# Optimization experiments

Hardware: AMD Instinct MI355X
Metric: run time of the kernel (lower is better)

The kernel has to match this reference:

```python
import jax, jax.numpy as jnp
import numpy as np

TOPK = 300
NUM_LEVELS = 3
GATE_TEMP = 1.0


def _normalized_grid(h, w):
    # matches torch: linspace(-1,1) meshgrid 'ij', stack (xx, yy) -> [h*w, 2]
    y = jnp.linspace(-1.0, 1.0, h, dtype=jnp.float32)
    x = jnp.linspace(-1.0, 1.0, w, dtype=jnp.float32)
    yy, xx = jnp.meshgrid(y, x, indexing='ij')
    return jnp.stack((xx, yy), axis=-1).reshape(h * w, 2)


def setup_inputs() -> dict:
    key = jax.random.key(0)
    ks = jax.random.split(key, 10)
    C, H_DIM, MAXL = 256, 256, 8
    shapes = [(8, C, 100, 152), (8, C, 50, 76), (8, C, 25, 38)]
    inp = {}
    for i, s in enumerate(shapes):
        inp[f'f{i}'] = jax.random.normal(ks[i], s, dtype=jnp.float32)
    inp['conv_w'] = jax.random.normal(ks[3], (C,), dtype=jnp.float32) * (1.0 / np.sqrt(C))
    inp['conv_b'] = jnp.zeros((1,), dtype=jnp.float32)
    inp['level_emb'] = jax.random.normal(ks[4], (MAXL, H_DIM), dtype=jnp.float32)
    qin = C + H_DIM + 3  # 515
    inp['w1'] = jax.random.normal(ks[5], (qin, H_DIM), dtype=jnp.float32) * (1.0 / np.sqrt(qin))
    inp['b1'] = jnp.zeros((H_DIM,), dtype=jnp.float32)
    inp['w2'] = jax.random.normal(ks[6], (H_DIM, H_DIM), dtype=jnp.float32) * (1.0 / np.sqrt(H_DIM))
    inp['b2'] = jnp.zeros((H_DIM,), dtype=jnp.float32)
    inp['gate_w'] = jax.random.normal(ks[7], (H_DIM, MAXL), dtype=jnp.float32) * (1.0 / np.sqrt(H_DIM))
    inp['gate_b'] = jnp.zeros((MAXL,), dtype=jnp.float32)
    inp['residual_scale'] = jnp.zeros((1,), dtype=jnp.float32)  # residual_scale_init=0.0
    return inp


def reference(f0, f1, f2, conv_w, conv_b, level_emb, w1, b1, w2, b2, gate_w, gate_b, residual_scale):
    levels = [f0, f1, f2]
    B = f0.shape[0]
    tok_s, tok_f, tok_p, tok_l = [], [], [], []
    for i, f in enumerate(levels):
        _, C, H, W = f.shape
        # 1x1 conv proxy objectness score -> [B, H*W]
        s = jnp.einsum('bchw,c->bhw', f, conv_w).reshape(B, H * W) + conv_b[0]
        tok_s.append(s)
        tok_f.append(f.reshape(B, C, H * W).transpose(0, 2, 1))       # [B, HW, C]
        tok_p.append(jnp.broadcast_to(_normalized_grid(H, W), (B, H * W, 2)))
        tok_l.append(jnp.full((B, H * W), i, dtype=jnp.int32))
    scores = jnp.concatenate(tok_s, axis=1)   # [B, N]
    feats = jnp.concatenate(tok_f, axis=1)    # [B, N, C]
    pos = jnp.concatenate(tok_p, axis=1)      # [B, N, 2]
    lvl = jnp.concatenate(tok_l, axis=1)      # [B, N]

    top_vals, top_idx = jax.lax.top_k(scores, TOPK)                     # [B, K]
    fk = jnp.take_along_axis(feats, top_idx[:, :, None], axis=1)        # [B, K, C]
    pk = jnp.take_along_axis(pos, top_idx[:, :, None], axis=1)          # [B, K, 2]
    lk = jnp.take_along_axis(lvl, top_idx, axis=1)                      # [B, K]
    sp = jax.nn.sigmoid(top_vals)                                       # [B, K]

    q = jnp.concatenate([fk, level_emb[lk], pk, sp[..., None]], axis=-1)  # [B, K, C+H+3]
    h = jax.nn.relu(q @ w1 + b1)
    h = jax.nn.relu(h @ w2 + b2)
    logits = (h @ gate_w + gate_b)[..., :NUM_LEVELS]                     # [B, K, L]
    gates = jax.nn.softmax(logits / GATE_TEMP, axis=-1)
    alpha = gates.mean(axis=1)                                           # [B, L]
    scale = 1.0 + residual_scale[0] * alpha                              # [B, L]

    outs = [f * scale[:, i][:, None, None, None] for i, f in enumerate(levels)]
    # flatten the output feature dict into one [B, sum(C*H*W)] array
    return jnp.concatenate([o.reshape(B, -1) for o in outs], axis=1)
```

## Files before the change

kernel.cpp:

```cpp
#include <hip/hip_runtime.h>
#include <hip/hip_bf16.h>

#define NTOK 19950
#define KTOP 300
#define NB 8
#define NQ (NB * KTOP)
#define QDIM 520

typedef float f32x4 __attribute__((ext_vector_type(4)));

__device__ __forceinline__ uint32_t fkey(float f) {
    uint32_t u = __float_as_uint(f);
    return (u & 0x80000000u) ? ~u : (u | 0x80000000u);
}

__global__ __launch_bounds__(256) void score_kernel(
    const float* __restrict__ f0, const float* __restrict__ f1, const float* __restrict__ f2,
    const float* __restrict__ conv_w, const float* __restrict__ conv_b,
    float* __restrict__ scores)
{
    __shared__ float cw[256];
    cw[threadIdx.x] = conv_w[threadIdx.x];
    __syncthreads();
    int t = blockIdx.x * 256 + threadIdx.x;
    if (t >= NB * NTOK) return;
    int b = t / NTOK;
    int pos = t - b * NTOK;
    const float* f; int HWl, hw;
    if (pos < 15200)      { f = f0; HWl = 15200; hw = pos; }
    else if (pos < 19000) { f = f1; HWl = 3800;  hw = pos - 15200; }
    else                  { f = f2; HWl = 950;   hw = pos - 19000; }
    const float* base = f + (size_t)b * 256 * HWl + hw;
    float s = 0.0f;
    #pragma unroll 16
    for (int c = 0; c < 256; ++c) s += base[(size_t)c * HWl] * cw[c];
    scores[t] = s + conv_b[0];
}

__global__ __launch_bounds__(1024, 1) void topk_kernel(
    const float* __restrict__ scores, int* __restrict__ top_idx)
{
    __shared__ uint32_t key[NTOK];
    __shared__ int whist[16][256];
    __shared__ int suffix[256];
    __shared__ uint32_t s_prefix;
    __shared__ int s_Kr, s_cnt, s_tcnt;
    __shared__ int tie[1024];
    const int tid = threadIdx.x;
    const int wv = tid >> 6;
    const int b = blockIdx.x;
    const float* srow = scores + b * NTOK;
    for (int i = tid; i < NTOK; i += 1024) key[i] = fkey(srow[i]);
    if (tid == 0) { s_prefix = 0u; s_Kr = KTOP; }
    __syncthreads();
    uint32_t pmask = 0u;
    for (int pass = 0; pass < 4; ++pass) {
        const int shift = 24 - 8 * pass;
        for (int i = tid; i < 16 * 256; i += 1024) ((int*)whist)[i] = 0;
        __syncthreads();
        const uint32_t prefix = s_prefix;
        const int Kr = s_Kr;
        for (int i = tid; i < NTOK; i += 1024) {
            uint32_t k = key[i];
            if ((k & pmask) == prefix) atomicAdd(&whist[wv][(k >> shift) & 255], 1);
        }
        __syncthreads();
        if (tid < 256) {
            int s = 0;
            #pragma unroll
            for (int w = 0; w < 16; ++w) s += whist[w][tid];
            suffix[tid] = s;
        }
        __syncthreads();
        for (int off = 1; off < 256; off <<= 1) {
            int t = 0;
            if (tid < 256 && tid + off < 256) t = suffix[tid + off];
            __syncthreads();
            if (tid < 256) suffix[tid] += t;
            __syncthreads();
        }
        if (tid < 256) {
            int sgeq = suffix[tid];
            int sgt  = (tid < 255) ? suffix[tid + 1] : 0;
            if (sgeq >= Kr && sgt < Kr) {
                s_prefix = prefix | ((uint32_t)tid << shift);
                s_Kr = Kr - sgt;
            }
        }
        __syncthreads();
        pmask |= (0xFFu << shift);
    }
    const uint32_t T = s_prefix;
    const int need = s_Kr;
    if (tid == 0) { s_cnt = 0; s_tcnt = 0; }
    __syncthreads();
    for (int i = tid; i < NTOK; i += 1024) {
        uint32_t k = key[i];
        if (k > T) {
            int p = atomicAdd(&s_cnt, 1);
            top_idx[b * KTOP + p] = i;
        } else if (k == T) {
            int p = atomicAdd(&s_tcnt, 1);
            if (p < 1024) tie[p] = i;
        }
    }
    __syncthreads();
    if (tid == 0) {
        int base = s_cnt;
        int tcnt = s_tcnt > 1024 ? 1024 : s_tcnt;
        for (int s = 0; s < need; ++s) {
            int mi = s;
            for (int u = s + 1; u < tcnt; ++u) if (tie[u] < tie[mi]) mi = u;
            int tmp = tie[s]; tie[s] = tie[mi]; tie[mi] = tmp;
            top_idx[b * KTOP + base + s] = tie[s];
        }
    }
}

__global__ __launch_bounds__(256) void gather_kernel(
    const float* __restrict__ f0, const float* __restrict__ f1, const float* __restrict__ f2,
    const float* __restrict__ scores, const int* __restrict__ top_idx,
    const float* __restrict__ level_emb, float* __restrict__ Q)
{
    const int k = blockIdx.x;
    const int b = k / KTOP;
    const int idx = top_idx[k];
    int lvl, hw, HWl, Wl, Hl;
    if (idx < 15200)      { lvl = 0; hw = idx;         HWl = 15200; Wl = 152; Hl = 100; }
    else if (idx < 19000) { lvl = 1; hw = idx - 15200; HWl = 3800;  Wl = 76;  Hl = 50;  }
    else                  { lvl = 2; hw = idx - 19000; HWl = 950;   Wl = 38;  Hl = 25;  }
    const float* f = (lvl == 0) ? f0 : ((lvl == 1) ? f1 : f2);
    const int c = threadIdx.x;
    float* qr = Q + (size_t)k * QDIM;
    qr[c]       = f[((size_t)b * 256 + c) * HWl + hw];
    qr[256 + c] = level_emb[lvl * 256 + c];
    if (c < 8) {
        float v = 0.0f;
        if (c == 0) {
            int hh = hw / Wl, ww = hw - hh * Wl;
            v = -1.0f + 2.0f * (float)ww / (float)(Wl - 1);
        } else if (c == 1) {
            int hh = hw / Wl;
            v = -1.0f + 2.0f * (float)hh / (float)(Hl - 1);
        } else if (c == 2) {
            float sv = scores[b * NTOK + idx];
            v = 1.0f / (1.0f + expf(-sv));
        }
        qr[512 + c] = v;
    }
}

#define QT 8
__global__ __launch_bounds__(512, 1) void mlp_kernel(
    const float* __restrict__ Q,
    const float* __restrict__ w1, const float* __restrict__ b1,
    const float* __restrict__ w2, const float* __restrict__ b2,
    const float* __restrict__ gate_w, const float* __restrict__ gate_b,
    float* __restrict__ G)
{
    __shared__ __align__(16) float q[QT][QDIM];
    __shared__ __align__(16) float part[QT][256];
    __shared__ __align__(16) float h[QT][256];
    const int tid = threadIdx.x;
    const int out = tid & 255;
    const int kh = tid >> 8;
    const int k0 = blockIdx.x * QT;

    {
        const float4* Qg = (const float4*)(Q + (size_t)k0 * QDIM);
        float4* qs = (float4*)&q[0][0];
        for (int i = tid; i < QT * QDIM / 4; i += 512) qs[i] = Qg[i];
    }
    __syncthreads();

    float acc[QT];

    {
        #pragma unroll
        for (int t = 0; t < QT; ++t) acc[t] = 0.0f;
        const float* wp = w1 + (size_t)(kh * 256) * 256 + out;
        float a0 = wp[0], a1 = wp[256], a2 = wp[512], a3 = wp[768];
        for (int i4 = 0; i4 < 64; ++i4) {
            float c0 = a0, c1 = a1, c2 = a2, c3 = a3;
            const float* wn = wp + 1024;
            if (i4 < 63) { a0 = wn[0]; a1 = wn[256]; a2 = wn[512]; a3 = wn[768]; }
            wp = wn;
            const int kb = kh * 256 + i4 * 4;
            #pragma unroll
            for (int t = 0; t < QT; ++t) {
                float4 qv = *reinterpret_cast<const float4*>(&q[t][kb]);
                acc[t] += qv.x * c0 + qv.y * c1 + qv.z * c2 + qv.w * c3;
            }
        }
        if (kh) {
            for (int r = 512; r < 515; ++r) {
                float wv = w1[(size_t)r * 256 + out];
                #pragma unroll
                for (int t = 0; t < QT; ++t) acc[t] += q[t][r] * wv;
            }
            #pragma unroll
            for (int t = 0; t < QT; ++t) part[t][out] = acc[t];
        }
    }
    __syncthreads();
    if (kh == 0) {
        float bj = b1[out];
        #pragma unroll
        for (int t = 0; t < QT; ++t) h[t][out] = fmaxf(acc[t] + part[t][out] + bj, 0.0f);
    }
    __syncthreads();

    {
        #pragma unroll
        for (int t = 0; t < QT; ++t) acc[t] = 0.0f;
        const float* wp = w2 + (size_t)(kh * 128) * 256 + out;
        float a0 = wp[0], a1 = wp[256], a2 = wp[512], a3 = wp[768];
        for (int i4 = 0; i4 < 32; ++i4) {
            float c0 = a0, c1 = a1, c2 = a2, c3 = a3;
            const float* wn = wp + 1024;
            if (i4 < 31) { a0 = wn[0]; a1 = wn[256]; a2 = wn[512]; a3 = wn[768]; }
            wp = wn;
            const int kb = kh * 128 + i4 * 4;
            #pragma unroll
            for (int t = 0; t < QT; ++t) {
                float4 hv = *reinterpret_cast<const float4*>(&h[t][kb]);
                acc[t] += hv.x * c0 + hv.y * c1 + hv.z * c2 + hv.w * c3;
            }
        }
        if (kh) {
            #pragma unroll
            for (int t = 0; t < QT; ++t) part[t][out] = acc[t];
        }
    }
    __syncthreads();
    if (kh == 0) {
        float bj = b2[out];
        #pragma unroll
        for (int t = 0; t < QT; ++t) q[t][out] = fmaxf(acc[t] + part[t][out] + bj, 0.0f);
    }
    __syncthreads();

    if (tid < 256) {
        const int t = tid >> 5, seg = tid & 31;
        float l0 = 0.f, l1 = 0.f, l2 = 0.f;
        for (int c = seg * 8; c < seg * 8 + 8; ++c) {
            float hv = q[t][c];
            l0 += hv * gate_w[c * 8 + 0];
            l1 += hv * gate_w[c * 8 + 1];
            l2 += hv * gate_w[c * 8 + 2];
        }
        float* gp = &part[0][0];
        gp[(t * 32 + seg) * 3 + 0] = l0;
        gp[(t * 32 + seg) * 3 + 1] = l1;
        gp[(t * 32 + seg) * 3 + 2] = l2;
    }
    __syncthreads();
    if (tid < QT) {
        const int t = tid;
        float l0 = gate_b[0], l1 = gate_b[1], l2 = gate_b[2];
        const float* gp = &part[0][0];
        for (int seg = 0; seg < 32; ++seg) {
            l0 += gp[(t * 32 + seg) * 3 + 0];
            l1 += gp[(t * 32 + seg) * 3 + 1];
            l2 += gp[(t * 32 + seg) * 3 + 2];
        }
        float m = fmaxf(l0, fmaxf(l1, l2));
        float e0 = expf(l0 - m), e1 = expf(l1 - m), e2 = expf(l2 - m);
        float inv = 1.0f / (e0 + e1 + e2);
        G[(k0 + t) * 3 + 0] = e0 * inv;
        G[(k0 + t) * 3 + 1] = e1 * inv;
        G[(k0 + t) * 3 + 2] = e2 * inv;
    }
}

__global__ void scale_kernel(const float* __restrict__ G,
                             const float* __restrict__ rs, float* __restrict__ scale)
{
    int tid = threadIdx.x;
    if (tid < NB * 3) {
        int b = tid / 3, l = tid % 3;
        float s = 0.0f;
        for (int k = 0; k < KTOP; ++k) s += G[(b * KTOP + k) * 3 + l];
        scale[tid] = 1.0f + rs[0] * (s / (float)KTOP);
    }
}

__global__ __launch_bounds__(256) void out_kernel(
    const f32x4* __restrict__ f0, const f32x4* __restrict__ f1, const f32x4* __restrict__ f2,
    const float* __restrict__ scale, f32x4* __restrict__ out)
{
    const int b = blockIdx.y;
    const int t0 = blockIdx.x * 256 + threadIdx.x;
    const int TPB = gridDim.x * 256;
    f32x4* ob = out + (size_t)b * 1276800;
    {
        const float sc = scale[b * 3 + 0];
        const f32x4* src = f0 + (size_t)b * 972800;
        for (int r = t0; r < 972800; r += TPB)
            __builtin_nontemporal_store(src[r] * sc, &ob[r]);
    }
    {
        const float sc = scale[b * 3 + 1];
        const f32x4* src = f1 + (size_t)b * 243200;
        f32x4* o1 = ob + 972800;
        for (int r = t0; r < 243200; r += TPB)
            __builtin_nontemporal_store(src[r] * sc, &o1[r]);
    }
    {
        const float sc = scale[b * 3 + 2];
        const f32x4* src = f2 + (size_t)b * 60800;
        f32x4* o2 = ob + 1216000;
        for (int r = t0; r < 60800; r += TPB)
            __builtin_nontemporal_store(src[r] * sc, &o2[r]);
    }
}

extern "C" void kernel_launch(void* const* d_in, const int* in_sizes, int n_in,
                              void* d_out, int out_size, void* d_ws, size_t ws_size,
                              hipStream_t stream)
{
    const float* f0        = (const float*)d_in[0];
    const float* f1        = (const float*)d_in[1];
    const float* f2        = (const float*)d_in[2];
    const float* conv_w    = (const float*)d_in[3];
    const float* conv_b    = (const float*)d_in[4];
    const float* level_emb = (const float*)d_in[5];
    const float* w1        = (const float*)d_in[6];
    const float* b1        = (const float*)d_in[7];
    const float* w2        = (const float*)d_in[8];
    const float* b2        = (const float*)d_in[9];
    const float* gate_w    = (const float*)d_in[10];
    const float* gate_b    = (const float*)d_in[11];
    const float* rs        = (const float*)d_in[12];

    char* ws = (char*)d_ws;
    float* scores   = (float*)ws;
    int*   top_idx  = (int*)(ws + 640 * 1024);
    float* G        = (float*)(ws + 656 * 1024);
    float* scale    = (float*)(ws + 688 * 1024);
    float* Q        = (float*)(ws + 704 * 1024);

    score_kernel<<<(NB * NTOK + 255) / 256, 256, 0, stream>>>(f0, f1, f2, conv_w, conv_b, scores);
    topk_kernel<<<NB, 1024, 0, stream>>>(scores, top_idx);
    gather_kernel<<<NQ, 256, 0, stream>>>(f0, f1, f2, scores, top_idx, level_emb, Q);
    mlp_kernel<<<NQ / QT, 512, 0, stream>>>(Q, w1, b1, w2, b2, gate_w, gate_b, G);
    scale_kernel<<<1, 32, 0, stream>>>(G, rs, scale);
    out_kernel<<<dim3(256, NB), 256, 0, stream>>>((const f32x4*)f0, (const f32x4*)f1,
                                                  (const f32x4*)f2, scale, (f32x4*)d_out);
}
```

Baseline: 167.2 us.

## Fuse gather into top-k, fold scale reduction into output kernel, vectorize scores

```diff
diff --git a/kernel.cpp b/kernel.cpp
--- a/kernel.cpp
+++ b/kernel.cpp
@@ -2,6 +2,7 @@
 #include <hip/hip_bf16.h>
 
 #define NTOK 19950
+#define NTOK2 9975
 #define KTOP 300
 #define NB 8
 #define NQ (NB * KTOP)
@@ -23,22 +24,30 @@
     cw[threadIdx.x] = conv_w[threadIdx.x];
     __syncthreads();
     int t = blockIdx.x * 256 + threadIdx.x;
-    if (t >= NB * NTOK) return;
-    int b = t / NTOK;
-    int pos = t - b * NTOK;
+    if (t >= NB * NTOK2) return;
+    int b = t / NTOK2;
+    int pos = (t - b * NTOK2) * 2;
     const float* f; int HWl, hw;
     if (pos < 15200)      { f = f0; HWl = 15200; hw = pos; }
     else if (pos < 19000) { f = f1; HWl = 3800;  hw = pos - 15200; }
     else                  { f = f2; HWl = 950;   hw = pos - 19000; }
-    const float* base = f + (size_t)b * 256 * HWl + hw;
-    float s = 0.0f;
+    const float2* base = (const float2*)(f + (size_t)b * 256 * HWl + hw);
+    const int stride2 = HWl >> 1;
+    float s0 = 0.0f, s1 = 0.0f;
     #pragma unroll 16
-    for (int c = 0; c < 256; ++c) s += base[(size_t)c * HWl] * cw[c];
-    scores[t] = s + conv_b[0];
-}
-
-__global__ __launch_bounds__(1024, 1) void topk_kernel(
-    const float* __restrict__ scores, int* __restrict__ top_idx)
+    for (int c = 0; c < 256; ++c) {
+        float2 v = base[(size_t)c * stride2];
+        s0 += v.x * cw[c];
+        s1 += v.y * cw[c];
+    }
+    scores[b * NTOK + pos]     = s0 + conv_b[0];
+    scores[b * NTOK + pos + 1] = s1 + conv_b[0];
+}
+
+__global__ __launch_bounds__(1024, 1) void topk_gather_kernel(
+    const float* __restrict__ scores,
+    const float* __restrict__ f0, const float* __restrict__ f1, const float* __restrict__ f2,
+    const float* __restrict__ level_emb, float* __restrict__ Q)
 {
     __shared__ uint32_t key[NTOK];
     __shared__ int whist[16][256];
@@ -46,6 +55,8 @@
     __shared__ uint32_t s_prefix;
     __shared__ int s_Kr, s_cnt, s_tcnt;
     __shared__ int tie[1024];
+    __shared__ int sel[KTOP];
+    __shared__ int g_lvl[KTOP], g_hw[KTOP], g_HW[KTOP];
     const int tid = threadIdx.x;
     const int wv = tid >> 6;
     const int b = blockIdx.x;
@@ -98,7 +109,7 @@
         uint32_t k = key[i];
         if (k > T) {
             int p = atomicAdd(&s_cnt, 1);
-            top_idx[b * KTOP + p] = i;
+            sel[p] = i;
         } else if (k == T) {
             int p = atomicAdd(&s_tcnt, 1);
             if (p < 1024) tie[p] = i;
@@ -112,41 +123,34 @@
             int mi = s;
             for (int u = s + 1; u < tcnt; ++u) if (tie[u] < tie[mi]) mi = u;
             int tmp = tie[s]; tie[s] = tie[mi]; tie[mi] = tmp;
-            top_idx[b * KTOP + base + s] = tie[s];
-        }
-    }
-}
-
-__global__ __launch_bounds__(256) void gather_kernel(
-    const float* __restrict__ f0, const float* __restrict__ f1, const float* __restrict__ f2,
-    const float* __restrict__ scores, const int* __restrict__ top_idx,
-    const float* __restrict__ level_emb, float* __restrict__ Q)
-{
-    const int k = blockIdx.x;
-    const int b = k / KTOP;
-    const int idx = top_idx[k];
-    int lvl, hw, HWl, Wl, Hl;
-    if (idx < 15200)      { lvl = 0; hw = idx;         HWl = 15200; Wl = 152; Hl = 100; }
-    else if (idx < 19000) { lvl = 1; hw = idx - 15200; HWl = 3800;  Wl = 76;  Hl = 50;  }
-    else                  { lvl = 2; hw = idx - 19000; HWl = 950;   Wl = 38;  Hl = 25;  }
-    const float* f = (lvl == 0) ? f0 : ((lvl == 1) ? f1 : f2);
-    const int c = threadIdx.x;
-    float* qr = Q + (size_t)k * QDIM;
-    qr[c]       = f[((size_t)b * 256 + c) * HWl + hw];
-    qr[256 + c] = level_emb[lvl * 256 + c];
-    if (c < 8) {
-        float v = 0.0f;
-        if (c == 0) {
-            int hh = hw / Wl, ww = hw - hh * Wl;
-            v = -1.0f + 2.0f * (float)ww / (float)(Wl - 1);
-        } else if (c == 1) {
-            int hh = hw / Wl;
-            v = -1.0f + 2.0f * (float)hh / (float)(Hl - 1);
-        } else if (c == 2) {
-            float sv = scores[b * NTOK + idx];
-            v = 1.0f / (1.0f + expf(-sv));
-        }
-        qr[512 + c] = v;
+            sel[base + s] = tie[s];
+        }
+    }
+    __syncthreads();
+    if (tid < KTOP) {
+        const int idx = sel[tid];
+        int lvl, hw, HWl, Wl, Hl;
+        if (idx < 15200)      { lvl = 0; hw = idx;         HWl = 15200; Wl = 152; Hl = 100; }
+        else if (idx < 19000) { lvl = 1; hw = idx - 15200; HWl = 3800;  Wl = 76;  Hl = 50;  }
+        else                  { lvl = 2; hw = idx - 19000; HWl = 950;   Wl = 38;  Hl = 25;  }
+        g_lvl[tid] = lvl; g_hw[tid] = hw; g_HW[tid] = HWl;
+        int hh = hw / Wl, ww = hw - hh * Wl;
+        float x = -1.0f + 2.0f * (float)ww / (float)(Wl - 1);
+        float y = -1.0f + 2.0f * (float)hh / (float)(Hl - 1);
+        float sv = srow[idx];
+        float sp = 1.0f / (1.0f + expf(-sv));
+        float* qr = Q + (size_t)(b * KTOP + tid) * QDIM;
+        qr[512] = x; qr[513] = y; qr[514] = sp;
+        qr[515] = 0.0f; qr[516] = 0.0f; qr[517] = 0.0f; qr[518] = 0.0f; qr[519] = 0.0f;
+    }
+    __syncthreads();
+    for (int j = tid; j < KTOP * 256; j += 1024) {
+        const int k = j >> 8, c = j & 255;
+        const int lvl = g_lvl[k];
+        const float* f = (lvl == 0) ? f0 : ((lvl == 1) ? f1 : f2);
+        float* qr = Q + (size_t)(b * KTOP + k) * QDIM;
+        qr[c]       = f[((size_t)b * 256 + c) * g_HW[k] + g_hw[k]];
+        qr[256 + c] = level_emb[lvl * 256 + c];
     }
 }
 
@@ -273,41 +277,51 @@
     }
 }
 
-__global__ void scale_kernel(const float* __restrict__ G,
-                             const float* __restrict__ rs, float* __restrict__ scale)
-{
-    int tid = threadIdx.x;
-    if (tid < NB * 3) {
-        int b = tid / 3, l = tid % 3;
-        float s = 0.0f;
-        for (int k = 0; k < KTOP; ++k) s += G[(b * KTOP + k) * 3 + l];
-        scale[tid] = 1.0f + rs[0] * (s / (float)KTOP);
-    }
-}
-
 __global__ __launch_bounds__(256) void out_kernel(
     const f32x4* __restrict__ f0, const f32x4* __restrict__ f1, const f32x4* __restrict__ f2,
-    const float* __restrict__ scale, f32x4* __restrict__ out)
-{
+    const float* __restrict__ G, const float* __restrict__ rs, f32x4* __restrict__ out)
+{
+    __shared__ float red[3][32];
+    __shared__ float ssc[3];
     const int b = blockIdx.y;
-    const int t0 = blockIdx.x * 256 + threadIdx.x;
+    const int tid = threadIdx.x;
+    if (tid < 96) {
+        const int l = tid / 32, c = tid % 32;
+        float s = 0.0f;
+        const int kb = c * 10;
+        const int ke = (kb + 10 < KTOP) ? kb + 10 : KTOP;
+        for (int k = kb; k < ke; ++k) s += G[(size_t)(b * KTOP + k) * 3 + l];
+        red[l][c] = s;
+    }
+    __syncthreads();
+    for (int off = 16; off > 0; off >>= 1) {
+        if (tid < 96) {
+            const int l = tid / 32, c = tid % 32;
+            if (c < off) red[l][c] += red[l][c + off];
+        }
+        __syncthreads();
+    }
+    if (tid < 3) ssc[tid] = 1.0f + rs[0] * (red[tid][0] / (float)KTOP);
+    __syncthreads();
+
+    const int t0 = blockIdx.x * 256 + tid;
     const int TPB = gridDim.x * 256;
     f32x4* ob = out + (size_t)b * 1276800;
     {
-        const float sc = scale[b * 3 + 0];
+        const float sc = ssc[0];
         const f32x4* src = f0 + (size_t)b * 972800;
         for (int r = t0; r < 972800; r += TPB)
             __builtin_nontemporal_store(src[r] * sc, &ob[r]);
     }
     {
-        const float sc = scale[b * 3 + 1];
+        const float sc = ssc[1];
         const f32x4* src = f1 + (size_t)b * 243200;
         f32x4* o1 = ob + 972800;
         for (int r = t0; r < 243200; r += TPB)
             __builtin_nontemporal_store(src[r] * sc, &o1[r]);
     }
     {
-        const float sc = scale[b * 3 + 2];
+        const float sc = ssc[2];
         const f32x4* src = f2 + (size_t)b * 60800;
         f32x4* o2 = ob + 1216000;
         for (int r = t0; r < 60800; r += TPB)
@@ -335,16 +349,13 @@
 
     char* ws = (char*)d_ws;
     float* scores   = (float*)ws;
-    int*   top_idx  = (int*)(ws + 640 * 1024);
     float* G        = (float*)(ws + 656 * 1024);
-    float* scale    = (float*)(ws + 688 * 1024);
     float* Q        = (float*)(ws + 704 * 1024);
 
-    score_kernel<<<(NB * NTOK + 255) / 256, 256, 0, stream>>>(f0, f1, f2, conv_w, conv_b, scores);
-    topk_kernel<<<NB, 1024, 0, stream>>>(scores, top_idx);
-    gather_kernel<<<NQ, 256, 0, stream>>>(f0, f1, f2, scores, top_idx, level_emb, Q);
+    score_kernel<<<(NB * NTOK2 + 255) / 256, 256, 0, stream>>>(
+        f0, f1, f2, conv_w, conv_b, scores);
+    topk_gather_kernel<<<NB, 1024, 0, stream>>>(scores, f0, f1, f2, level_emb, Q);
     mlp_kernel<<<NQ / QT, 512, 0, stream>>>(Q, w1, b1, w2, b2, gate_w, gate_b, G);
-    scale_kernel<<<1, 32, 0, stream>>>(G, rs, scale);
     out_kernel<<<dim3(256, NB), 256, 0, stream>>>((const f32x4*)f0, (const f32x4*)f1,
-                                                  (const f32x4*)f2, scale, (f32x4*)d_out);
-}
+                                                  (const f32x4*)f2, G, rs, (f32x4*)d_out);
+}
```

New measurement: 247.5 us. +48.0%, slower.
